# Optimization experiments

Hardware: AMD Instinct MI355X
Metric: run time of the kernel (lower is better)

## Reference

```python
import jax, jax.numpy as jnp
import numpy as np

B, T = 256, 4096
L = 128          # shapelet_length
K = 128          # num_shapelets
K_TOP = 5


def setup_inputs() -> dict:
    key = jax.random.key(0)
    kx, ks = jax.random.split(key)
    x = jax.random.normal(kx, (B, T), dtype=jnp.float32)
    shapelets = jax.random.normal(ks, (K, L), dtype=jnp.float32) * 0.1
    return {"x": x, "shapelets": shapelets}


def reference(x, shapelets):
    # x: [B, T], shapelets: [K, L]
    N = x.shape[1] - L + 1  # number of sliding windows
    # Gather overlapping windows: x_win [B, N, L]
    idx = jnp.arange(N)[:, None] + jnp.arange(L)[None, :]
    x_win = x[:, idx]
    # Per-window mean removal
    x_norm = x_win - jnp.mean(x_win, axis=2, keepdims=True)
    # Per-shapelet mean removal
    s_norm = shapelets - jnp.mean(shapelets, axis=1, keepdims=True)
    # Correlation: [B, N, K]
    corr = jnp.einsum('bnl,kl->bnk', x_norm, s_norm)
    k_val = min(K_TOP, N)
    # top-k over window dim N -> move N to last axis
    topk_vals, _ = jax.lax.top_k(jnp.transpose(corr, (0, 2, 1)), k_val)  # [B, K, k]
    p1 = topk_vals[:, :, 0]
    p2 = topk_vals[:, :, 1] if k_val >= 2 else p1
    p_mean = jnp.mean(topk_vals, axis=2)
    dominance = jax.nn.relu(p1 - p2)
    return jnp.concatenate([p1, p_mean, p2, dominance], axis=1)  # [B, 4K]
```

## Files before the change

kernel.cpp:

```cpp
#include <hip/hip_runtime.h>

#define T_LEN 4096
#define N_WIN 3969
#define K_SH  128
#define L_SH  128
#define B_SZ  256

#define SSTR  136
#define XSTR  4360

typedef __attribute__((ext_vector_type(8))) __bf16 bf16x8;
typedef __attribute__((ext_vector_type(4))) float f32x4;
typedef _Float16 h2 __attribute__((ext_vector_type(2)));

__device__ __forceinline__ unsigned short f2bf(float f) {
    union { float f; unsigned int u; } c; c.f = f;
    unsigned int u = c.u + 0x7fff + ((c.u >> 16) & 1u);
    return (unsigned short)(u >> 16);
}
__device__ __forceinline__ unsigned int pack2(unsigned short lo, unsigned short hi) {
    return (unsigned int)lo | ((unsigned int)hi << 16);
}

__device__ __forceinline__ h2 max2(h2 a, h2 b) { return __builtin_elementwise_max(a, b); }
__device__ __forceinline__ h2 min2(h2 a, h2 b) { return __builtin_elementwise_min(a, b); }
__device__ __forceinline__ h2 cvt2(float lo, float hi) {
    return __builtin_bit_cast(h2, __builtin_amdgcn_cvt_pkrtz(lo, hi));
}
__device__ __forceinline__ void ce2(h2& hi, h2& lo) {
    const h2 m = max2(hi, lo);
    lo = min2(hi, lo);
    hi = m;
}
__device__ __forceinline__ void sort4_2(h2& a, h2& b, h2& c, h2& d) {
    ce2(a, b); ce2(c, d); ce2(a, c); ce2(b, d); ce2(b, c);
}
__device__ __forceinline__ void merge44_top5_2(h2 a0, h2 a1, h2 a2, h2 a3,
                                               h2 b0, h2 b1, h2 b2, h2 b3,
                                               h2& r0, h2& r1, h2& r2, h2& r3, h2& r4) {
    ce2(a0, b0); ce2(a2, b2); ce2(b0, a2);
    ce2(a1, b1); ce2(a3, b3); ce2(b1, a3);
    r0 = a0;
    r1 = a1; r2 = b0; ce2(r1, r2);
    r3 = b1; r4 = a2; ce2(r3, r4);
}
__device__ __forceinline__ void merge55_2(h2& r0, h2& r1, h2& r2, h2& r3, h2& r4,
                                          h2 s0, h2 s1, h2 s2, h2 s3, h2 s4) {
    const h2 m00 = min2(r0, s0);
    const h2 m10 = min2(r1, s0), m01 = min2(r0, s1);
    const h2 m20 = min2(r2, s0), m11 = min2(r1, s1), m02 = min2(r0, s2);
    const h2 m30 = min2(r3, s0), m21 = min2(r2, s1), m12 = min2(r1, s2), m03 = min2(r0, s3);
    const h2 n0 = max2(r0, s0);
    const h2 n1 = max2(max2(r1, s1), m00);
    const h2 n2 = max2(max2(r2, s2), max2(m10, m01));
    const h2 n3 = max2(max2(max2(r3, s3), m20), max2(m11, m02));
    const h2 n4 = max2(max2(max2(r4, s4), max2(m30, m03)), max2(m21, m12));
    r0 = n0; r1 = n1; r2 = n2; r3 = n3; r4 = n4;
}
__device__ __forceinline__ void insert1_2(h2 v, h2* rt) {
    h2 b = max2(rt[4], v); h2 m;
    m = max2(rt[3], b);     b     = min2(rt[3], b);     rt[3] = m;
    m = max2(rt[2], rt[3]); rt[3] = min2(rt[2], rt[3]); rt[2] = m;
    m = max2(rt[1], rt[2]); rt[2] = min2(rt[1], rt[2]); rt[1] = m;
    m = max2(rt[0], rt[1]); rt[1] = min2(rt[0], rt[1]); rt[0] = m;
    rt[4] = b;
}
__device__ __forceinline__ void select32(const f32x4* acc0, const f32x4* acc1, h2* rt) {
    h2 p[16];
    #pragma unroll
    for (int m = 0; m < 4; ++m)
        #pragma unroll
        for (int i = 0; i < 4; ++i)
            p[4 * m + i] = cvt2(acc0[m][i], acc1[m][i]);
    sort4_2(p[0], p[1], p[2],  p[3]);
    sort4_2(p[4], p[5], p[6],  p[7]);
    sort4_2(p[8], p[9], p[10], p[11]);
    sort4_2(p[12], p[13], p[14], p[15]);
    h2 u0, u1, u2, u3, u4, v0, v1, v2, v3, v4;
    merge44_top5_2(p[0], p[1], p[2],  p[3],  p[4],  p[5],  p[6],  p[7],  u0, u1, u2, u3, u4);
    merge44_top5_2(p[8], p[9], p[10], p[11], p[12], p[13], p[14], p[15], v0, v1, v2, v3, v4);
    merge55_2(u0, u1, u2, u3, u4, v0, v1, v2, v3, v4);
    merge55_2(rt[0], rt[1], rt[2], rt[3], rt[4], u0, u1, u2, u3, u4);
}

__global__ __launch_bounds__(1024)
void shapelet_fused_kernel(const float* __restrict__ x,
                           const float* __restrict__ s,
                           float* __restrict__ out) {
    __shared__ __align__(16) unsigned short ldsS[K_SH * SSTR];
    __shared__ __align__(16) unsigned short ldsX[8 * XSTR];

    const int t    = threadIdx.x;
    const int lane = t & 63;
    const int w    = t >> 6;
    const int r    = lane & 15;
    const int q    = lane >> 4;
    const int c7   = lane & 7;
    const int ub   = (lane >> 3) & 1;
    const int g    = w >> 3;
    const int w7   = w & 7;
    const int mh   = w7 >> 2;
    const int wp   = w7 & 3;
    const int mtb  = 4 * mh;
    const int b    = blockIdx.x;

    {
        const int k = t >> 3, e8 = t & 7;
        const float4* srow = (const float4*)(s + k * L_SH + e8 * 16);
        float4 v[4];
        float sum = 0.0f;
        #pragma unroll
        for (int j = 0; j < 4; ++j) {
            v[j] = srow[j];
            sum += (v[j].x + v[j].y) + (v[j].z + v[j].w);
        }
        sum += __shfl_xor(sum, 1);
        sum += __shfl_xor(sum, 2);
        sum += __shfl_xor(sum, 4);
        const float mean = sum * (1.0f / 128.0f);
        uint4* dst = (uint4*)((char*)ldsS + k * (SSTR * 2) + e8 * 32);
        #pragma unroll
        for (int j = 0; j < 2; ++j) {
            uint4 o;
            o.x = pack2(f2bf(v[2*j].x - mean),   f2bf(v[2*j].y - mean));
            o.y = pack2(f2bf(v[2*j].z - mean),   f2bf(v[2*j].w - mean));
            o.z = pack2(f2bf(v[2*j+1].x - mean), f2bf(v[2*j+1].y - mean));
            o.w = pack2(f2bf(v[2*j+1].z - mean), f2bf(v[2*j+1].w - mean));
            dst[j] = o;
        }
        if (e8 == 7) *(uint4*)((char*)ldsS + k * (SSTR * 2) + 256) = make_uint4(0,0,0,0);
    }

    {
        const float* __restrict__ xb = x + (size_t)b * T_LEN;
        const int a = t & 7;
        for (int i = (t >> 3); i < XSTR / 8; i += 128) {
            const int p0 = 8 * i;
            float xv[16];
            if (p0 + 16 <= T_LEN) {
                const float4* sp = (const float4*)(xb + p0);
                #pragma unroll
                for (int j = 0; j < 4; ++j) *(float4*)(xv + 4 * j) = sp[j];
            } else {
                #pragma unroll
                for (int j = 0; j < 16; ++j) {
                    const int gi = p0 + j;
                    xv[j] = (gi < T_LEN) ? xb[gi] : 0.0f;
                }
            }
            unsigned short bv[16];
            #pragma unroll
            for (int j = 0; j < 16; ++j) bv[j] = f2bf(xv[j]);
            uint4 o;
            o.x = pack2(bv[a],     bv[a + 1]);
            o.y = pack2(bv[a + 2], bv[a + 3]);
            o.z = pack2(bv[a + 4], bv[a + 5]);
            o.w = pack2(bv[a + 6], bv[a + 7]);
            *(uint4*)((char*)ldsX + a * (XSTR * 2) + 2 * p0) = o;
        }
    }
    __syncthreads();

    bf16x8 bfr[2][4];
    #pragma unroll
    for (int kk = 0; kk < 2; ++kk)
        #pragma unroll
        for (int c = 0; c < 4; ++c)
            bfr[kk][c] = __builtin_bit_cast(bf16x8, *(const uint4*)(
                (const char*)ldsS + ((2 * wp + kk) * 16 + r) * (SSTR * 2) + 64 * c + 16 * q));

    h2 rt[5];
    #pragma unroll
    for (int i = 0; i < 5; ++i) rt[i] = __builtin_bit_cast(h2, 0xFC00FC00u);

    const char* xp = (const char*)ldsX + c7 * (XSTR * 2) + 16 * q + 16 * ub + 32 * mtb
                   + g * 256;

#define TILE_STEP                                                               \
    {                                                                           \
        bf16x8 afr[10];                                                         \
        _Pragma("unroll")                                                       \
        for (int j = 0; j < 10; ++j)                                            \
            afr[j] = __builtin_bit_cast(bf16x8, *(const uint4*)(xp + 32 * j));  \
        xp += 512;                                                              \
        f32x4 acc0[4], acc1[4];                                                 \
        _Pragma("unroll")                                                       \
        for (int m = 0; m < 4; ++m) {                                           \
            acc0[m] = (f32x4){0.f, 0.f, 0.f, 0.f};                              \
            acc1[m] = (f32x4){0.f, 0.f, 0.f, 0.f};                              \
        }                                                                       \
        _Pragma("unroll")                                                       \
        for (int c = 0; c < 4; ++c) {                                           \
            _Pragma("unroll")                                                   \
            for (int m = 0; m < 4; ++m) {                                       \
                acc0[m] = __builtin_amdgcn_mfma_f32_16x16x32_bf16(afr[m + 2*c], bfr[0][c], acc0[m], 0, 0, 0); \
                acc1[m] = __builtin_amdgcn_mfma_f32_16x16x32_bf16(afr[m + 2*c], bfr[1][c], acc1[m], 0, 0, 0); \
            }                                                                   \
        }                                                                       \
        select32(acc0, acc1, rt);                                               \
    }

    for (int st = 0; st < 15; ++st) { TILE_STEP }
    if (g == 0) { TILE_STEP }
#undef TILE_STEP

    if (g == 1 && mh == 0) {
        f32x4 e0 = (f32x4){0.f, 0.f, 0.f, 0.f};
        f32x4 e1 = (f32x4){0.f, 0.f, 0.f, 0.f};
        const char* eb = (const char*)ldsX + c7 * (XSTR * 2) + 7936 + 16 * q + 16 * ub;
        #pragma unroll
        for (int c = 0; c < 4; ++c) {
            const bf16x8 af = __builtin_bit_cast(bf16x8, *(const uint4*)(eb + 64 * c));
            e0 = __builtin_amdgcn_mfma_f32_16x16x32_bf16(af, bfr[0][c], e0, 0, 0, 0);
            e1 = __builtin_amdgcn_mfma_f32_16x16x32_bf16(af, bfr[1][c], e1, 0, 0, 0);
        }
        if (q == 0) insert1_2(cvt2(e0[0], e1[0]), rt);
    }

    #pragma unroll
    for (int mask = 16; mask <= 32; mask <<= 1) {
        h2 sv[5];
        #pragma unroll
        for (int i = 0; i < 5; ++i)
            sv[i] = __builtin_bit_cast(h2, __shfl_xor(__builtin_bit_cast(int, rt[i]), mask));
        merge55_2(rt[0], rt[1], rt[2], rt[3], rt[4], sv[0], sv[1], sv[2], sv[3], sv[4]);
    }

    __syncthreads();
    unsigned int* pbuf = (unsigned int*)ldsS;
    if ((g != 0 || mh != 0) && q == 0) {
        const int reg = (g * 2 + mh) - 1;
        unsigned int* p = pbuf + ((reg * 64) + wp * 16 + r) * 5;
        #pragma unroll
        for (int i = 0; i < 5; ++i) p[i] = __builtin_bit_cast(unsigned int, rt[i]);
    }
    __syncthreads();
    if (g == 0 && mh == 0 && q == 0) {
        #pragma unroll
        for (int reg = 0; reg < 3; ++reg) {
            const unsigned int* p = pbuf + ((reg * 64) + wp * 16 + r) * 5;
            h2 sv[5];
            #pragma unroll
            for (int i = 0; i < 5; ++i) sv[i] = __builtin_bit_cast(h2, p[i]);
            merge55_2(rt[0], rt[1], rt[2], rt[3], rt[4], sv[0], sv[1], sv[2], sv[3], sv[4]);
        }

        const float A0 = (float)rt[0][0], A1 = (float)rt[1][0], A2 = (float)rt[2][0],
                    A3 = (float)rt[3][0], A4 = (float)rt[4][0];
        const float B0 = (float)rt[0][1], B1 = (float)rt[1][1], B2 = (float)rt[2][1],
                    B3 = (float)rt[3][1], B4 = (float)rt[4][1];
        float* ob = out + (size_t)b * (4 * K_SH);
        const int ksA = 32 * wp + r, ksB = ksA + 16;
        const float mA = (((A0 + A1) + (A2 + A3)) + A4) * 0.2f;
        const float mB = (((B0 + B1) + (B2 + B3)) + B4) * 0.2f;
        ob[ksA]           = A0;
        ob[K_SH + ksA]    = mA;
        ob[2*K_SH + ksA]  = A1;
        ob[3*K_SH + ksA]  = fmaxf(A0 - A1, 0.0f);
        ob[ksB]           = B0;
        ob[K_SH + ksB]    = mB;
        ob[2*K_SH + ksB]  = B1;
        ob[3*K_SH + ksB]  = fmaxf(B0 - B1, 0.0f);
    }
}

extern "C" void kernel_launch(void* const* d_in, const int* in_sizes, int n_in,
                              void* d_out, int out_size, void* d_ws, size_t ws_size,
                              hipStream_t stream) {
    const float* x = (const float*)d_in[0];
    const float* s = (const float*)d_in[1];
    float* out = (float*)d_out;
    shapelet_fused_kernel<<<B_SZ, 1024, 0, stream>>>(x, s, out);
}
```

Before: 94.70 us.

## Split each batch row's windows across two blocks and merge top-5 in second kernel

Each batch row is now handled by two blocks, each covering half of the time series, so the grid grows from 256 to 512 blocks. This should fill more of the device's compute units and shrink the LDS footprint per block. Each block writes its partial top-5 lists to workspace, and a small second kernel merges the two halves and writes the final features. The cost is an extra kernel launch, a round trip through global memory for the partials, and the shared-shapelet preprocessing being redone in twice as many blocks.

```diff
diff --git a/kernel.cpp b/kernel.cpp
--- a/kernel.cpp
+++ b/kernel.cpp
@@ -7,7 +7,7 @@
 #define B_SZ  256
 
 #define SSTR  136
-#define XSTR  4360
+#define XSTRH 2248
 
 typedef __attribute__((ext_vector_type(8))) __bf16 bf16x8;
 typedef __attribute__((ext_vector_type(4))) float f32x4;
@@ -83,12 +83,12 @@
     merge55_2(rt[0], rt[1], rt[2], rt[3], rt[4], u0, u1, u2, u3, u4);
 }
 
-__global__ __launch_bounds__(1024)
-void shapelet_fused_kernel(const float* __restrict__ x,
-                           const float* __restrict__ s,
-                           float* __restrict__ out) {
+__global__ __launch_bounds__(1024, 8)
+void shapelet_half_kernel(const float* __restrict__ x,
+                          const float* __restrict__ s,
+                          unsigned int* __restrict__ part) {
     __shared__ __align__(16) unsigned short ldsS[K_SH * SSTR];
-    __shared__ __align__(16) unsigned short ldsX[8 * XSTR];
+    __shared__ __align__(16) unsigned short ldsX[8 * XSTRH];
 
     const int t    = threadIdx.x;
     const int lane = t & 63;
@@ -102,7 +102,8 @@
     const int mh   = w7 >> 2;
     const int wp   = w7 & 3;
     const int mtb  = 4 * mh;
-    const int b    = blockIdx.x;
+    const int half = blockIdx.x & 1;
+    const int b    = blockIdx.x >> 1;
 
     {
         const int k = t >> 3, e8 = t & 7;
@@ -132,12 +133,13 @@
     }
 
     {
-        const float* __restrict__ xb = x + (size_t)b * T_LEN;
+        const float* __restrict__ xb = x + (size_t)b * T_LEN + half * 2048;
+        const int navail = half ? 2048 : 2175;
         const int a = t & 7;
-        for (int i = (t >> 3); i < XSTR / 8; i += 128) {
+        for (int i = (t >> 3); i < XSTRH / 8; i += 128) {
             const int p0 = 8 * i;
             float xv[16];
-            if (p0 + 16 <= T_LEN) {
+            if (p0 + 16 <= 2048) {
                 const float4* sp = (const float4*)(xb + p0);
                 #pragma unroll
                 for (int j = 0; j < 4; ++j) *(float4*)(xv + 4 * j) = sp[j];
@@ -145,7 +147,7 @@
                 #pragma unroll
                 for (int j = 0; j < 16; ++j) {
                     const int gi = p0 + j;
-                    xv[j] = (gi < T_LEN) ? xb[gi] : 0.0f;
+                    xv[j] = (gi < navail) ? xb[gi] : 0.0f;
                 }
             }
             unsigned short bv[16];
@@ -156,7 +158,7 @@
             o.y = pack2(bv[a + 2], bv[a + 3]);
             o.z = pack2(bv[a + 4], bv[a + 5]);
             o.w = pack2(bv[a + 6], bv[a + 7]);
-            *(uint4*)((char*)ldsX + a * (XSTR * 2) + 2 * p0) = o;
+            *(uint4*)((char*)ldsX + a * (XSTRH * 2) + 2 * p0) = o;
         }
     }
     __syncthreads();
@@ -173,7 +175,7 @@
     #pragma unroll
     for (int i = 0; i < 5; ++i) rt[i] = __builtin_bit_cast(h2, 0xFC00FC00u);
 
-    const char* xp = (const char*)ldsX + c7 * (XSTR * 2) + 16 * q + 16 * ub + 32 * mtb
+    const char* xp = (const char*)ldsX + c7 * (XSTRH * 2) + 16 * q + 16 * ub + 32 * mtb
                    + g * 256;
 
 #define TILE_STEP                                                               \
@@ -200,14 +202,14 @@
         select32(acc0, acc1, rt);                                               \
     }
 
-    for (int st = 0; st < 15; ++st) { TILE_STEP }
-    if (g == 0) { TILE_STEP }
+    for (int st = 0; st < 7; ++st) { TILE_STEP }
+    if (!(half & g)) { TILE_STEP }
 #undef TILE_STEP
 
-    if (g == 1 && mh == 0) {
+    if (half == 1 && g == 1 && mh == 0) {
         f32x4 e0 = (f32x4){0.f, 0.f, 0.f, 0.f};
         f32x4 e1 = (f32x4){0.f, 0.f, 0.f, 0.f};
-        const char* eb = (const char*)ldsX + c7 * (XSTR * 2) + 7936 + 16 * q + 16 * ub;
+        const char* eb = (const char*)ldsX + c7 * (XSTRH * 2) + 3840 + 16 * q + 16 * ub;
         #pragma unroll
         for (int c = 0; c < 4; ++c) {
             const bf16x8 af = __builtin_bit_cast(bf16x8, *(const uint4*)(eb + 64 * c));
@@ -244,24 +246,43 @@
             for (int i = 0; i < 5; ++i) sv[i] = __builtin_bit_cast(h2, p[i]);
             merge55_2(rt[0], rt[1], rt[2], rt[3], rt[4], sv[0], sv[1], sv[2], sv[3], sv[4]);
         }
-
-        const float A0 = (float)rt[0][0], A1 = (float)rt[1][0], A2 = (float)rt[2][0],
-                    A3 = (float)rt[3][0], A4 = (float)rt[4][0];
-        const float B0 = (float)rt[0][1], B1 = (float)rt[1][1], B2 = (float)rt[2][1],
-                    B3 = (float)rt[3][1], B4 = (float)rt[4][1];
-        float* ob = out + (size_t)b * (4 * K_SH);
-        const int ksA = 32 * wp + r, ksB = ksA + 16;
-        const float mA = (((A0 + A1) + (A2 + A3)) + A4) * 0.2f;
-        const float mB = (((B0 + B1) + (B2 + B3)) + B4) * 0.2f;
-        ob[ksA]           = A0;
-        ob[K_SH + ksA]    = mA;
-        ob[2*K_SH + ksA]  = A1;
-        ob[3*K_SH + ksA]  = fmaxf(A0 - A1, 0.0f);
-        ob[ksB]           = B0;
-        ob[K_SH + ksB]    = mB;
-        ob[2*K_SH + ksB]  = B1;
-        ob[3*K_SH + ksB]  = fmaxf(B0 - B1, 0.0f);
-    }
+        const int cid = wp * 16 + r;
+        unsigned int* p = part + (size_t)(half * 5) * 16384 + b * 64 + cid;
+        #pragma unroll
+        for (int j = 0; j < 5; ++j)
+            p[(size_t)j * 16384] = __builtin_bit_cast(unsigned int, rt[j]);
+    }
+}
+
+__global__ void merge_half_kernel(const unsigned int* __restrict__ part,
+                                  float* __restrict__ out) {
+    const int gid = blockIdx.x * 256 + threadIdx.x;
+    const int b   = gid >> 6;
+    const int cid = gid & 63;
+
+    h2 rt[5], sv[5];
+    #pragma unroll
+    for (int j = 0; j < 5; ++j) rt[j] = __builtin_bit_cast(h2, part[(size_t)j * 16384 + gid]);
+    #pragma unroll
+    for (int j = 0; j < 5; ++j) sv[j] = __builtin_bit_cast(h2, part[(size_t)(5 + j) * 16384 + gid]);
+    merge55_2(rt[0], rt[1], rt[2], rt[3], rt[4], sv[0], sv[1], sv[2], sv[3], sv[4]);
+
+    const float A0 = (float)rt[0][0], A1 = (float)rt[1][0], A2 = (float)rt[2][0],
+                A3 = (float)rt[3][0], A4 = (float)rt[4][0];
+    const float B0 = (float)rt[0][1], B1 = (float)rt[1][1], B2 = (float)rt[2][1],
+                B3 = (float)rt[3][1], B4 = (float)rt[4][1];
+    float* ob = out + (size_t)b * (4 * K_SH);
+    const int ksA = 32 * (cid >> 4) + (cid & 15), ksB = ksA + 16;
+    const float mA = (((A0 + A1) + (A2 + A3)) + A4) * 0.2f;
+    const float mB = (((B0 + B1) + (B2 + B3)) + B4) * 0.2f;
+    ob[ksA]           = A0;
+    ob[K_SH + ksA]    = mA;
+    ob[2*K_SH + ksA]  = A1;
+    ob[3*K_SH + ksA]  = fmaxf(A0 - A1, 0.0f);
+    ob[ksB]           = B0;
+    ob[K_SH + ksB]    = mB;
+    ob[2*K_SH + ksB]  = B1;
+    ob[3*K_SH + ksB]  = fmaxf(B0 - B1, 0.0f);
 }
 
 extern "C" void kernel_launch(void* const* d_in, const int* in_sizes, int n_in,
@@ -270,5 +291,8 @@
     const float* x = (const float*)d_in[0];
     const float* s = (const float*)d_in[1];
     float* out = (float*)d_out;
-    shapelet_fused_kernel<<<B_SZ, 1024, 0, stream>>>(x, s, out);
-}
+    unsigned int* part = (unsigned int*)d_ws;
+
+    shapelet_half_kernel<<<2 * B_SZ, 1024, 0, stream>>>(x, s, part);
+    merge_half_kernel<<<64, 256, 0, stream>>>(part, out);
+}
```

New measurement: 146.2 us. +54.4%, slower.

## Switch to 32x32x16 MFMA tiles with double-buffered accumulators and fp32 final merge

Applied to the files above, without the earlier changes.

Replaces the 16x16x32 bf16 MFMA tiling with 32x32x16 MFMAs, so each wave owns 32 shapelets and both packed half-lanes of the selection network hold windows rather than shapelets. Two sets of accumulators alternate so the top-5 selection of one tile can overlap the MFMAs of the next tile. The cross-lane and cross-wave reductions are reworked to merge in fp32 with fewer shuffle stages. The aim is fewer MFMA issues and fewer LDS A-fragment loads per output, at the cost of higher register pressure from four 16-wide accumulators.

```diff
diff --git a/kernel.cpp b/kernel.cpp
--- a/kernel.cpp
+++ b/kernel.cpp
@@ -9,8 +9,10 @@
 #define SSTR  136
 #define XSTR  4360
 
+#define NEG_INF (-3.402823466e38f)
+
 typedef __attribute__((ext_vector_type(8))) __bf16 bf16x8;
-typedef __attribute__((ext_vector_type(4))) float f32x4;
+typedef __attribute__((ext_vector_type(16))) float f32x16;
 typedef _Float16 h2 __attribute__((ext_vector_type(2)));
 
 __device__ __forceinline__ unsigned short f2bf(float f) {
@@ -57,24 +59,36 @@
     const h2 n4 = max2(max2(max2(r4, s4), max2(m30, m03)), max2(m21, m12));
     r0 = n0; r1 = n1; r2 = n2; r3 = n3; r4 = n4;
 }
-__device__ __forceinline__ void insert1_2(h2 v, h2* rt) {
-    h2 b = max2(rt[4], v); h2 m;
-    m = max2(rt[3], b);     b     = min2(rt[3], b);     rt[3] = m;
-    m = max2(rt[2], rt[3]); rt[3] = min2(rt[2], rt[3]); rt[2] = m;
-    m = max2(rt[1], rt[2]); rt[2] = min2(rt[1], rt[2]); rt[1] = m;
-    m = max2(rt[0], rt[1]); rt[1] = min2(rt[0], rt[1]); rt[0] = m;
-    rt[4] = b;
-}
-__device__ __forceinline__ void select32(const f32x4* acc0, const f32x4* acc1, h2* rt) {
+__device__ __forceinline__ void merge55f(float& r0, float& r1, float& r2, float& r3, float& r4,
+                                         float s0, float s1, float s2, float s3, float s4) {
+    const float m00 = fminf(r0, s0);
+    const float m10 = fminf(r1, s0), m01 = fminf(r0, s1);
+    const float m20 = fminf(r2, s0), m11 = fminf(r1, s1), m02 = fminf(r0, s2);
+    const float m30 = fminf(r3, s0), m21 = fminf(r2, s1), m12 = fminf(r1, s2), m03 = fminf(r0, s3);
+    const float n0 = fmaxf(r0, s0);
+    const float n1 = fmaxf(fmaxf(r1, s1), m00);
+    const float n2 = fmaxf(fmaxf(r2, s2), fmaxf(m10, m01));
+    const float n3 = fmaxf(fmaxf(fmaxf(r3, s3), m20), fmaxf(m11, m02));
+    const float n4 = fmaxf(fmaxf(fmaxf(r4, s4), fmaxf(m30, m03)), fmaxf(m21, m12));
+    r0 = n0; r1 = n1; r2 = n2; r3 = n3; r4 = n4;
+}
+__device__ __forceinline__ void top5_insertf(float v, float& t0, float& t1,
+                                             float& t2, float& t3, float& t4) {
+    float b = fmaxf(t4, v);
+    float m;
+    m = fmaxf(t3, b);  b  = fminf(t3, b);  t3 = m;
+    m = fmaxf(t2, t3); t3 = fminf(t2, t3); t2 = m;
+    m = fmaxf(t1, t2); t2 = fminf(t1, t2); t1 = m;
+    m = fmaxf(t0, t1); t1 = fminf(t0, t1); t0 = m;
+    t4 = b;
+}
+__device__ __forceinline__ void select32b(const f32x16& A0, const f32x16& A1, h2* rt) {
     h2 p[16];
     #pragma unroll
-    for (int m = 0; m < 4; ++m)
-        #pragma unroll
-        for (int i = 0; i < 4; ++i)
-            p[4 * m + i] = cvt2(acc0[m][i], acc1[m][i]);
-    sort4_2(p[0], p[1], p[2],  p[3]);
-    sort4_2(p[4], p[5], p[6],  p[7]);
-    sort4_2(p[8], p[9], p[10], p[11]);
+    for (int i = 0; i < 16; ++i) p[i] = cvt2(A0[i], A1[i]);
+    sort4_2(p[0],  p[1],  p[2],  p[3]);
+    sort4_2(p[4],  p[5],  p[6],  p[7]);
+    sort4_2(p[8],  p[9],  p[10], p[11]);
     sort4_2(p[12], p[13], p[14], p[15]);
     h2 u0, u1, u2, u3, u4, v0, v1, v2, v3, v4;
     merge44_top5_2(p[0], p[1], p[2],  p[3],  p[4],  p[5],  p[6],  p[7],  u0, u1, u2, u3, u4);
@@ -93,15 +107,13 @@
     const int t    = threadIdx.x;
     const int lane = t & 63;
     const int w    = t >> 6;
-    const int r    = lane & 15;
-    const int q    = lane >> 4;
     const int c7   = lane & 7;
-    const int ub   = (lane >> 3) & 1;
+    const int ub2  = (lane >> 3) & 3;
+    const int q2   = lane >> 5;
+    const int col  = lane & 31;
     const int g    = w >> 3;
-    const int w7   = w & 7;
-    const int mh   = w7 >> 2;
-    const int wp   = w7 & 3;
-    const int mtb  = 4 * mh;
+    const int mp   = (w >> 2) & 1;
+    const int kt   = w & 3;
     const int b    = blockIdx.x;
 
     {
@@ -161,106 +173,111 @@
     }
     __syncthreads();
 
-    bf16x8 bfr[2][4];
+    bf16x8 bfr[8];
     #pragma unroll
-    for (int kk = 0; kk < 2; ++kk)
-        #pragma unroll
-        for (int c = 0; c < 4; ++c)
-            bfr[kk][c] = __builtin_bit_cast(bf16x8, *(const uint4*)(
-                (const char*)ldsS + ((2 * wp + kk) * 16 + r) * (SSTR * 2) + 64 * c + 16 * q));
+    for (int c = 0; c < 8; ++c)
+        bfr[c] = __builtin_bit_cast(bf16x8, *(const uint4*)(
+            (const char*)ldsS + (32 * kt + col) * (SSTR * 2) + 32 * c + 16 * q2));
 
     h2 rt[5];
     #pragma unroll
     for (int i = 0; i < 5; ++i) rt[i] = __builtin_bit_cast(h2, 0xFC00FC00u);
 
-    const char* xp = (const char*)ldsX + c7 * (XSTR * 2) + 16 * q + 16 * ub + 32 * mtb
-                   + g * 256;
-
-#define TILE_STEP                                                               \
+    const char* xp = (const char*)ldsX + c7 * (XSTR * 2) + 16 * ub2 + 16 * q2
+                   + 128 * mp + g * 256;
+
+    f32x16 aA0, aA1, aB0, aB1;
+
+#define LD(U) __builtin_bit_cast(bf16x8, *(const uint4*)(xp + 32 * (U)))
+#define COMPUTE(X0, X1)                                                         \
     {                                                                           \
-        bf16x8 afr[10];                                                         \
         _Pragma("unroll")                                                       \
-        for (int j = 0; j < 10; ++j)                                            \
-            afr[j] = __builtin_bit_cast(bf16x8, *(const uint4*)(xp + 32 * j));  \
+        for (int i = 0; i < 16; ++i) { X0[i] = 0.f; X1[i] = 0.f; }              \
+        bf16x8 f;                                                               \
+        f = LD(0); X0 = __builtin_amdgcn_mfma_f32_32x32x16_bf16(f, bfr[0], X0, 0, 0, 0); \
+        f = LD(1); X0 = __builtin_amdgcn_mfma_f32_32x32x16_bf16(f, bfr[1], X0, 0, 0, 0); \
+        f = LD(2); X0 = __builtin_amdgcn_mfma_f32_32x32x16_bf16(f, bfr[2], X0, 0, 0, 0); \
+                   X1 = __builtin_amdgcn_mfma_f32_32x32x16_bf16(f, bfr[0], X1, 0, 0, 0); \
+        f = LD(3); X0 = __builtin_amdgcn_mfma_f32_32x32x16_bf16(f, bfr[3], X0, 0, 0, 0); \
+                   X1 = __builtin_amdgcn_mfma_f32_32x32x16_bf16(f, bfr[1], X1, 0, 0, 0); \
+        f = LD(4); X0 = __builtin_amdgcn_mfma_f32_32x32x16_bf16(f, bfr[4], X0, 0, 0, 0); \
+                   X1 = __builtin_amdgcn_mfma_f32_32x32x16_bf16(f, bfr[2], X1, 0, 0, 0); \
+        f = LD(5); X0 = __builtin_amdgcn_mfma_f32_32x32x16_bf16(f, bfr[5], X0, 0, 0, 0); \
+                   X1 = __builtin_amdgcn_mfma_f32_32x32x16_bf16(f, bfr[3], X1, 0, 0, 0); \
+        f = LD(6); X0 = __builtin_amdgcn_mfma_f32_32x32x16_bf16(f, bfr[6], X0, 0, 0, 0); \
+                   X1 = __builtin_amdgcn_mfma_f32_32x32x16_bf16(f, bfr[4], X1, 0, 0, 0); \
+        f = LD(7); X0 = __builtin_amdgcn_mfma_f32_32x32x16_bf16(f, bfr[7], X0, 0, 0, 0); \
+                   X1 = __builtin_amdgcn_mfma_f32_32x32x16_bf16(f, bfr[5], X1, 0, 0, 0); \
+        f = LD(8); X1 = __builtin_amdgcn_mfma_f32_32x32x16_bf16(f, bfr[6], X1, 0, 0, 0); \
+        f = LD(9); X1 = __builtin_amdgcn_mfma_f32_32x32x16_bf16(f, bfr[7], X1, 0, 0, 0); \
         xp += 512;                                                              \
-        f32x4 acc0[4], acc1[4];                                                 \
-        _Pragma("unroll")                                                       \
-        for (int m = 0; m < 4; ++m) {                                           \
-            acc0[m] = (f32x4){0.f, 0.f, 0.f, 0.f};                              \
-            acc1[m] = (f32x4){0.f, 0.f, 0.f, 0.f};                              \
-        }                                                                       \
-        _Pragma("unroll")                                                       \
-        for (int c = 0; c < 4; ++c) {                                           \
-            _Pragma("unroll")                                                   \
-            for (int m = 0; m < 4; ++m) {                                       \
-                acc0[m] = __builtin_amdgcn_mfma_f32_16x16x32_bf16(afr[m + 2*c], bfr[0][c], acc0[m], 0, 0, 0); \
-                acc1[m] = __builtin_amdgcn_mfma_f32_16x16x32_bf16(afr[m + 2*c], bfr[1][c], acc1[m], 0, 0, 0); \
-            }                                                                   \
-        }                                                                       \
-        select32(acc0, acc1, rt);                                               \
-    }
-
-    for (int st = 0; st < 15; ++st) { TILE_STEP }
-    if (g == 0) { TILE_STEP }
-#undef TILE_STEP
-
-    if (g == 1 && mh == 0) {
-        f32x4 e0 = (f32x4){0.f, 0.f, 0.f, 0.f};
-        f32x4 e1 = (f32x4){0.f, 0.f, 0.f, 0.f};
-        const char* eb = (const char*)ldsX + c7 * (XSTR * 2) + 7936 + 16 * q + 16 * ub;
-        #pragma unroll
-        for (int c = 0; c < 4; ++c) {
-            const bf16x8 af = __builtin_bit_cast(bf16x8, *(const uint4*)(eb + 64 * c));
-            e0 = __builtin_amdgcn_mfma_f32_16x16x32_bf16(af, bfr[0][c], e0, 0, 0, 0);
-            e1 = __builtin_amdgcn_mfma_f32_16x16x32_bf16(af, bfr[1][c], e1, 0, 0, 0);
-        }
-        if (q == 0) insert1_2(cvt2(e0[0], e1[0]), rt);
-    }
-
-    #pragma unroll
-    for (int mask = 16; mask <= 32; mask <<= 1) {
-        h2 sv[5];
-        #pragma unroll
-        for (int i = 0; i < 5; ++i)
-            sv[i] = __builtin_bit_cast(h2, __shfl_xor(__builtin_bit_cast(int, rt[i]), mask));
-        merge55_2(rt[0], rt[1], rt[2], rt[3], rt[4], sv[0], sv[1], sv[2], sv[3], sv[4]);
+    }
+
+    COMPUTE(aA0, aA1)
+    for (int st = 0; st < 7; ++st) {
+        COMPUTE(aB0, aB1) select32b(aA0, aA1, rt);
+        COMPUTE(aA0, aA1) select32b(aB0, aB1, rt);
+    }
+    if (g == 0) {
+        COMPUTE(aB0, aB1) select32b(aA0, aA1, rt);
+        select32b(aB0, aB1, rt);
+    } else {
+        select32b(aA0, aA1, rt);
+    }
+#undef COMPUTE
+#undef LD
+
+    f32x16 eb;
+    if (g == 1 && mp == 0) {
+        #pragma unroll
+        for (int i = 0; i < 16; ++i) eb[i] = 0.f;
+        const char* ebase = (const char*)ldsX + c7 * (XSTR * 2) + 16 * ub2 + 16 * q2 + 7936;
+        #pragma unroll
+        for (int c = 0; c < 8; ++c) {
+            const bf16x8 f = __builtin_bit_cast(bf16x8, *(const uint4*)(ebase + 32 * c));
+            eb = __builtin_amdgcn_mfma_f32_32x32x16_bf16(f, bfr[c], eb, 0, 0, 0);
+        }
+    }
+
+    float a0 = (float)rt[0][0], a1 = (float)rt[1][0], a2 = (float)rt[2][0],
+          a3 = (float)rt[3][0], a4 = (float)rt[4][0];
+    merge55f(a0, a1, a2, a3, a4,
+             (float)rt[0][1], (float)rt[1][1], (float)rt[2][1],
+             (float)rt[3][1], (float)rt[4][1]);
+
+    if (g == 1 && mp == 0) {
+        const float v = (q2 == 0) ? eb[0] : NEG_INF;
+        top5_insertf(v, a0, a1, a2, a3, a4);
+    }
+
+    {
+        const float s0 = __shfl_xor(a0, 32), s1 = __shfl_xor(a1, 32),
+                    s2 = __shfl_xor(a2, 32), s3 = __shfl_xor(a3, 32),
+                    s4 = __shfl_xor(a4, 32);
+        merge55f(a0, a1, a2, a3, a4, s0, s1, s2, s3, s4);
     }
 
     __syncthreads();
-    unsigned int* pbuf = (unsigned int*)ldsS;
-    if ((g != 0 || mh != 0) && q == 0) {
-        const int reg = (g * 2 + mh) - 1;
-        unsigned int* p = pbuf + ((reg * 64) + wp * 16 + r) * 5;
-        #pragma unroll
-        for (int i = 0; i < 5; ++i) p[i] = __builtin_bit_cast(unsigned int, rt[i]);
+    float* sc = (float*)ldsS;
+    const int slot = 2 * g + mp;
+    if (slot != 0 && lane < 32) {
+        float* p = sc + (((slot - 1) * 128) + kt * 32 + col) * 5;
+        p[0] = a0; p[1] = a1; p[2] = a2; p[3] = a3; p[4] = a4;
     }
     __syncthreads();
-    if (g == 0 && mh == 0 && q == 0) {
-        #pragma unroll
-        for (int reg = 0; reg < 3; ++reg) {
-            const unsigned int* p = pbuf + ((reg * 64) + wp * 16 + r) * 5;
-            h2 sv[5];
-            #pragma unroll
-            for (int i = 0; i < 5; ++i) sv[i] = __builtin_bit_cast(h2, p[i]);
-            merge55_2(rt[0], rt[1], rt[2], rt[3], rt[4], sv[0], sv[1], sv[2], sv[3], sv[4]);
-        }
-
-        const float A0 = (float)rt[0][0], A1 = (float)rt[1][0], A2 = (float)rt[2][0],
-                    A3 = (float)rt[3][0], A4 = (float)rt[4][0];
-        const float B0 = (float)rt[0][1], B1 = (float)rt[1][1], B2 = (float)rt[2][1],
-                    B3 = (float)rt[3][1], B4 = (float)rt[4][1];
+    if (slot == 0 && lane < 32) {
+        #pragma unroll
+        for (int sreg = 0; sreg < 3; ++sreg) {
+            const float* p = sc + ((sreg * 128) + kt * 32 + col) * 5;
+            merge55f(a0, a1, a2, a3, a4, p[0], p[1], p[2], p[3], p[4]);
+        }
+        const int ks = 32 * kt + col;
         float* ob = out + (size_t)b * (4 * K_SH);
-        const int ksA = 32 * wp + r, ksB = ksA + 16;
-        const float mA = (((A0 + A1) + (A2 + A3)) + A4) * 0.2f;
-        const float mB = (((B0 + B1) + (B2 + B3)) + B4) * 0.2f;
-        ob[ksA]           = A0;
-        ob[K_SH + ksA]    = mA;
-        ob[2*K_SH + ksA]  = A1;
-        ob[3*K_SH + ksA]  = fmaxf(A0 - A1, 0.0f);
-        ob[ksB]           = B0;
-        ob[K_SH + ksB]    = mB;
-        ob[2*K_SH + ksB]  = B1;
-        ob[3*K_SH + ksB]  = fmaxf(B0 - B1, 0.0f);
+        const float pmean = (((a0 + a1) + (a2 + a3)) + a4) * 0.2f;
+        ob[ks]            = a0;
+        ob[K_SH + ks]     = pmean;
+        ob[2*K_SH + ks]   = a1;
+        ob[3*K_SH + ks]   = fmaxf(a0 - a1, 0.0f);
     }
 }
 
```

After: 100.5 us. 6.1% more time.
